# Performance work log

Hardware: AMD Instinct MI355X
Metric: run time of the kernel (lower is better)

The kernel has to match this reference:

```python
import jax, jax.numpy as jnp
import numpy as np

OUT_F, IN_F = 4096, 4096
BITS = 4
B, S = 4, 2048


def setup_inputs() -> dict:
    key = jax.random.key(0)
    k_x, k_cb, k_rot, k_b, k_idx = jax.random.split(key, 5)
    x = jax.random.normal(k_x, (B, S, IN_F), dtype=jnp.float32)
    # per-coordinate codebook indices for each weight row (int, constant)
    indices = jax.random.randint(k_idx, (OUT_F, IN_F), 0, 2 ** BITS, dtype=jnp.int32)
    # scalar codebook with 2^bits levels
    codebook = jax.random.normal(k_cb, (2 ** BITS,), dtype=jnp.float32)
    # random rotation Pi (d x d); faithful math only needs it orthogonal-ish
    rotation_matrix = jax.random.normal(k_rot, (IN_F, IN_F), dtype=jnp.float32) / np.sqrt(IN_F)
    bias = jax.random.normal(k_b, (OUT_F,), dtype=jnp.float32)
    return {"x": x, "indices": indices, "codebook": codebook,
            "rotation_matrix": rotation_matrix, "bias": bias}


def reference(x, indices, codebook, rotation_matrix, bias):
    # Dequantize: look up codewords per coordinate in rotated space, then
    # undo the rotation: W = C[idx] @ Pi^T  -> [out_features, in_features]
    rotated = codebook[indices]                      # [O, D] gather
    weight = jnp.einsum('od,kd->ok', rotated, rotation_matrix)  # rotated @ Pi^T
    # F.linear(x, W, bias) = x @ W^T + bias
    out = jnp.einsum('bsd,od->bso', x, weight) + bias
    return out
```

## Files before the change

kernel.cpp:

```cpp
#include <hip/hip_runtime.h>
#include <hip/hip_bf16.h>


typedef __attribute__((ext_vector_type(8))) __bf16 bf16x8;
typedef __attribute__((ext_vector_type(4))) float f32x4;

#define GLOAD_LDS16(g, l)                                                        \
  __builtin_amdgcn_global_load_lds((__attribute__((address_space(1))) void*)(g), \
                                   (__attribute__((address_space(3))) void*)(l), \
                                   16, 0, 0)

#define SB() __builtin_amdgcn_sched_barrier(0)


__global__ __launch_bounds__(256) void cvt_f32_bf16(const float* __restrict__ in,
                                                    __hip_bfloat16* __restrict__ out, int n4) {
  int i = blockIdx.x * 256 + threadIdx.x;
  if (i >= n4) return;
  float4 v = *(const float4*)(in + (size_t)i * 4);
  union { __hip_bfloat16 h[4]; ushort4 u; } o;
  o.h[0] = __float2bfloat16(v.x);
  o.h[1] = __float2bfloat16(v.y);
  o.h[2] = __float2bfloat16(v.z);
  o.h[3] = __float2bfloat16(v.w);
  *(ushort4*)((unsigned short*)out + (size_t)i * 4) = o.u;
}

__global__ __launch_bounds__(256) void dequant_bf16(const int* __restrict__ idx,
                                                    const float* __restrict__ cb,
                                                    __hip_bfloat16* __restrict__ out, int n4) {
  __shared__ __hip_bfloat16 scb[16];
  if (threadIdx.x < 16) scb[threadIdx.x] = __float2bfloat16(cb[threadIdx.x]);
  __syncthreads();
  int i = blockIdx.x * 256 + threadIdx.x;
  if (i >= n4) return;
  int4 v = *(const int4*)(idx + (size_t)i * 4);
  union { __hip_bfloat16 h[4]; ushort4 u; } o;
  o.h[0] = scb[v.x & 15];
  o.h[1] = scb[v.y & 15];
  o.h[2] = scb[v.z & 15];
  o.h[3] = scb[v.w & 15];
  *(ushort4*)((unsigned short*)out + (size_t)i * 4) = o.u;
}


template <bool OUT_BF16>
__global__ __launch_bounds__(512, 2) void gemm256(const __hip_bfloat16* __restrict__ A,
                                                  const __hip_bfloat16* __restrict__ B,
                                                  void* __restrict__ Cv,
                                                  const float* __restrict__ bias,
                                                  int M, int N, int K) {
  __shared__ __align__(16) char smem[131072];

  const int nbn = N >> 8;
  const int nwg = (M >> 8) * nbn;
  const int bid0 = blockIdx.x;
  const int cpx = nwg >> 3;
  const int bid = (bid0 & 7) * cpx + (bid0 >> 3);
  const int m0 = (bid / nbn) << 8;
  const int n0 = (bid % nbn) << 8;

  const int tid = (int)threadIdx.x;
  const int lane = tid & 63;
  const int w = tid >> 6;
  const int wr = w >> 2;
  const int wc = w & 3;
  const int fr = lane & 15;
  const int fq = lane >> 4;

  const int srow = lane >> 3;
  const int scol = ((lane & 7) ^ srow) << 3;

  const __hip_bfloat16* Ab = A + (size_t)m0 * K;
  const __hip_bfloat16* Bb = B + (size_t)n0 * K;

  const int NT = K >> 6;

  f32x4 acc[8][4];
#pragma unroll
  for (int i = 0; i < 8; ++i)
#pragma unroll
    for (int j = 0; j < 4; ++j) acc[i][j] = (f32x4){0.f, 0.f, 0.f, 0.f};

  auto stage = [&](int s) {
    const int t = s >> 2, kind = s & 3;
    const __hip_bfloat16* g = (kind < 2) ? Ab : Bb;
    char* region = smem + ((kind < 2) ? 0 : 65536) + (t & 1) * 32768 + (kind & 1) * 16384;
    const int grow = (kind & 1) * 128 + w * 16 + srow;
    const int k0 = t << 6;
#pragma unroll
    for (int j = 0; j < 2; ++j)
      GLOAD_LDS16(g + (size_t)(grow + j * 8) * K + (k0 + scol), region + w * 2048 + j * 1024);
  };

  const int fr2 = (fr >> 2) & 1;
  const int fcol = (fq ^ (fr & 3)) << 4;
  const char* pA0 = smem + wr * 16384 + fr * 128 + fcol + 64 * fr2;
  const char* pA1 = smem + wr * 16384 + fr * 128 + fcol + 64 * (1 - fr2);
  const char* pB0 = smem + 65536 + wc * 8192 + fr * 128 + fcol + 64 * fr2;
  const char* pB1 = smem + 65536 + wc * 8192 + fr * 128 + fcol + 64 * (1 - fr2);

#define LDA(BUF, MH, MF, KK) \
  (*(const bf16x8*)(((KK) ? pA1 : pA0) + (BUF) * 32768 + (MH) * 8192 + (MF) * 2048))
#define LDB(BUF, NF, KK) (*(const bf16x8*)(((KK) ? pB1 : pB0) + (BUF) * 32768 + (NF) * 2048))

  stage(0); stage(1); stage(2); stage(3);
  stage(6); stage(7);

  bf16x8 afA[4], afB[4], bk0[4], bk1[4];

#define TILE_BODY(BUF, T)                                                                     \
  {                                                                                           \
    const bool pf1 = ((T) + 1 < NT);                                                          \
    const bool pf2 = ((T) + 2 < NT);                                                          \
                  \
    if ((T) + 1 == NT) {                                                                      \
      asm volatile("s_waitcnt vmcnt(0)" ::: "memory");                                        \
    } else {                                                                                  \
      asm volatile("s_waitcnt vmcnt(4)" ::: "memory");                                        \
    }                                                                                         \
    __builtin_amdgcn_s_barrier();                                                             \
    _Pragma("unroll") for (int mf = 0; mf < 4; ++mf) afA[mf] = LDA(BUF, 0, mf, 0);            \
    _Pragma("unroll") for (int nf = 0; nf < 4; ++nf) bk0[nf] = LDB(BUF, nf, 0);               \
    if (pf1) stage(4 * ((T) + 1) + 0);                                                        \
    asm volatile("s_waitcnt lgkmcnt(0)");                                                     \
    SB();                                                                                     \
    _Pragma("unroll") for (int nf = 0; nf < 4; ++nf)                                          \
        _Pragma("unroll") for (int mf = 0; mf < 4; ++mf)                                      \
            acc[mf][nf] =                                                                     \
                __builtin_amdgcn_mfma_f32_16x16x32_bf16(afA[mf], bk0[nf], acc[mf][nf], 0, 0, 0); \
                                    \
    _Pragma("unroll") for (int mf = 0; mf < 4; ++mf) afB[mf] = LDA(BUF, 0, mf, 1);            \
    _Pragma("unroll") for (int nf = 0; nf < 4; ++nf) bk1[nf] = LDB(BUF, nf, 1);               \
    __builtin_amdgcn_s_barrier();                                                             \
    if (pf1) stage(4 * ((T) + 1) + 1);                                                        \
    asm volatile("s_waitcnt lgkmcnt(0)");                                                     \
    SB();                                                                                     \
    _Pragma("unroll") for (int nf = 0; nf < 4; ++nf)                                          \
        _Pragma("unroll") for (int mf = 0; mf < 4; ++mf)                                      \
            acc[mf][nf] =                                                                     \
                __builtin_amdgcn_mfma_f32_16x16x32_bf16(afB[mf], bk1[nf], acc[mf][nf], 0, 0, 0); \
          \
    _Pragma("unroll") for (int mf = 0; mf < 4; ++mf) afA[mf] = LDA(BUF, 1, mf, 0);            \
    _Pragma("unroll") for (int mf = 0; mf < 4; ++mf) afB[mf] = LDA(BUF, 1, mf, 1);            \
    __builtin_amdgcn_s_barrier();                                                             \
    if (pf2) {                                                                                \
      stage(4 * ((T) + 2) + 2);                                                               \
      stage(4 * ((T) + 2) + 3);                                                               \
    }                                                                                         \
    asm volatile("s_waitcnt lgkmcnt(0)");                                                     \
    SB();                                                                                     \
    _Pragma("unroll") for (int nf = 0; nf < 4; ++nf)                                          \
        _Pragma("unroll") for (int mf = 0; mf < 4; ++mf)                                      \
            acc[4 + mf][nf] = __builtin_amdgcn_mfma_f32_16x16x32_bf16(afA[mf], bk0[nf],       \
                                                                      acc[4 + mf][nf], 0, 0, 0); \
    _Pragma("unroll") for (int nf = 0; nf < 4; ++nf)                                          \
        _Pragma("unroll") for (int mf = 0; mf < 4; ++mf)                                      \
            acc[4 + mf][nf] = __builtin_amdgcn_mfma_f32_16x16x32_bf16(afB[mf], bk1[nf],       \
                                                                      acc[4 + mf][nf], 0, 0, 0); \
  }

  for (int T = 0; T < NT; T += 2) {
    TILE_BODY(0, T);
    TILE_BODY(1, T + 1);
  }
#undef TILE_BODY
#undef LDA
#undef LDB

  if constexpr (OUT_BF16) {
    __hip_bfloat16* C = (__hip_bfloat16*)Cv;
#pragma unroll
    for (int mi = 0; mi < 8; ++mi)
#pragma unroll
      for (int ni = 0; ni < 4; ++ni) {
        const size_t row = (size_t)(m0 + wr * 128 + (mi >> 2) * 64 + (mi & 3) * 16 + fq * 4);
        const int col = n0 + wc * 64 + ni * 16 + fr;
#pragma unroll
        for (int v = 0; v < 4; ++v) C[(row + v) * N + col] = __float2bfloat16(acc[mi][ni][v]);
      }
  } else {
    float* C = (float*)Cv;
    float bv[4];
#pragma unroll
    for (int ni = 0; ni < 4; ++ni) bv[ni] = bias[n0 + wc * 64 + ni * 16 + fr];
#pragma unroll
    for (int mi = 0; mi < 8; ++mi)
#pragma unroll
      for (int ni = 0; ni < 4; ++ni) {
        const size_t row = (size_t)(m0 + wr * 128 + (mi >> 2) * 64 + (mi & 3) * 16 + fq * 4);
        const int col = n0 + wc * 64 + ni * 16 + fr;
#pragma unroll
        for (int v = 0; v < 4; ++v) C[(row + v) * N + col] = acc[mi][ni][v] + bv[ni];
      }
  }
}


extern "C" void kernel_launch(void* const* d_in, const int* in_sizes, int n_in,
                              void* d_out, int out_size, void* d_ws, size_t ws_size,
                              hipStream_t stream) {
  const float* x = (const float*)d_in[0];
  const int* indices = (const int*)d_in[1];
  const float* codebook = (const float*)d_in[2];
  const float* rot = (const float*)d_in[3];
  const float* bias = (const float*)d_in[4];
  float* out = (float*)d_out;

  const int D = 4096, O = 4096;
  const int M = in_sizes[0] / D;

  char* ws = (char*)d_ws;
  __hip_bfloat16* Xb = (__hip_bfloat16*)ws;
  __hip_bfloat16* Rb = (__hip_bfloat16*)(ws + ((size_t)64 << 20));
  __hip_bfloat16* Wr = (__hip_bfloat16*)(ws + ((size_t)96 << 20));
  __hip_bfloat16* Wb = (__hip_bfloat16*)(ws + ((size_t)128 << 20));

  cvt_f32_bf16<<<(M * D / 4 + 255) / 256, 256, 0, stream>>>(x, Xb, M * D / 4);
  cvt_f32_bf16<<<(4096 * 4096 / 4 + 255) / 256, 256, 0, stream>>>(rot, Rb, 4096 * 4096 / 4);
  dequant_bf16<<<(4096 * 4096 / 4 + 255) / 256, 256, 0, stream>>>(indices, codebook, Wr,
                                                                  4096 * 4096 / 4);

  gemm256<true><<<dim3((O / 256) * (4096 / 256)), 512, 0, stream>>>(Wr, Rb, Wb, nullptr, O, 4096,
                                                                    D);
  gemm256<false><<<dim3((M / 256) * (O / 256)), 512, 0, stream>>>(Xb, Wb, out, bias, M, O, 4096);
}
```

Before: 415.5 us.

## Replace 256x256 GEMM tile with 128x128 tile and simpler pipeline

Shrinks each GEMM workgroup from a 256x256 output tile with 8 waves to a 128x128 tile with 4 waves, halves LDS use, and simplifies the prefetch schedule: a full vmcnt(0) wait, then all four stages of the next tile issued at once. This gives more workgroups and higher occupancy, but lowers per-tile data reuse, roughly doubles global/LDS traffic per FLOP, and drops the staggered prefetch overlap.

```diff
diff --git a/kernel.cpp b/kernel.cpp
--- a/kernel.cpp
+++ b/kernel.cpp
@@ -45,26 +45,26 @@
 
 
 template <bool OUT_BF16>
-__global__ __launch_bounds__(512, 2) void gemm256(const __hip_bfloat16* __restrict__ A,
+__global__ __launch_bounds__(256, 2) void gemm128(const __hip_bfloat16* __restrict__ A,
                                                   const __hip_bfloat16* __restrict__ B,
                                                   void* __restrict__ Cv,
                                                   const float* __restrict__ bias,
                                                   int M, int N, int K) {
-  __shared__ __align__(16) char smem[131072];
-
-  const int nbn = N >> 8;
-  const int nwg = (M >> 8) * nbn;
+  __shared__ __align__(16) char smem[65536];
+
+  const int nbn = N >> 7;
+  const int nwg = (M >> 7) * nbn;
   const int bid0 = blockIdx.x;
   const int cpx = nwg >> 3;
   const int bid = (bid0 & 7) * cpx + (bid0 >> 3);
-  const int m0 = (bid / nbn) << 8;
-  const int n0 = (bid % nbn) << 8;
+  const int m0 = (bid / nbn) << 7;
+  const int n0 = (bid % nbn) << 7;
 
   const int tid = (int)threadIdx.x;
   const int lane = tid & 63;
   const int w = tid >> 6;
-  const int wr = w >> 2;
-  const int wc = w & 3;
+  const int wr = w >> 1;
+  const int wc = w & 1;
   const int fr = lane & 15;
   const int fq = lane >> 4;
 
@@ -76,17 +76,17 @@
 
   const int NT = K >> 6;
 
-  f32x4 acc[8][4];
-#pragma unroll
-  for (int i = 0; i < 8; ++i)
+  f32x4 acc[4][4];
+#pragma unroll
+  for (int i = 0; i < 4; ++i)
 #pragma unroll
     for (int j = 0; j < 4; ++j) acc[i][j] = (f32x4){0.f, 0.f, 0.f, 0.f};
 
   auto stage = [&](int s) {
     const int t = s >> 2, kind = s & 3;
     const __hip_bfloat16* g = (kind < 2) ? Ab : Bb;
-    char* region = smem + ((kind < 2) ? 0 : 65536) + (t & 1) * 32768 + (kind & 1) * 16384;
-    const int grow = (kind & 1) * 128 + w * 16 + srow;
+    char* region = smem + ((kind < 2) ? 0 : 32768) + (t & 1) * 16384 + (kind & 1) * 8192;
+    const int grow = (kind & 1) * 64 + w * 16 + srow;
     const int k0 = t << 6;
 #pragma unroll
     for (int j = 0; j < 2; ++j)
@@ -95,69 +95,47 @@
 
   const int fr2 = (fr >> 2) & 1;
   const int fcol = (fq ^ (fr & 3)) << 4;
-  const char* pA0 = smem + wr * 16384 + fr * 128 + fcol + 64 * fr2;
-  const char* pA1 = smem + wr * 16384 + fr * 128 + fcol + 64 * (1 - fr2);
-  const char* pB0 = smem + 65536 + wc * 8192 + fr * 128 + fcol + 64 * fr2;
-  const char* pB1 = smem + 65536 + wc * 8192 + fr * 128 + fcol + 64 * (1 - fr2);
-
-#define LDA(BUF, MH, MF, KK) \
-  (*(const bf16x8*)(((KK) ? pA1 : pA0) + (BUF) * 32768 + (MH) * 8192 + (MF) * 2048))
-#define LDB(BUF, NF, KK) (*(const bf16x8*)(((KK) ? pB1 : pB0) + (BUF) * 32768 + (NF) * 2048))
+  const char* pA0 = smem + wr * 8192 + fr * 128 + fcol + 64 * fr2;
+  const char* pA1 = smem + wr * 8192 + fr * 128 + fcol + 64 * (1 - fr2);
+  const char* pB0 = smem + 32768 + wc * 8192 + fr * 128 + fcol + 64 * fr2;
+  const char* pB1 = smem + 32768 + wc * 8192 + fr * 128 + fcol + 64 * (1 - fr2);
+
+#define LDA(BUF, MF, KK) (*(const bf16x8*)(((KK) ? pA1 : pA0) + (BUF) * 16384 + (MF) * 2048))
+#define LDB(BUF, NF, KK) (*(const bf16x8*)(((KK) ? pB1 : pB0) + (BUF) * 16384 + (NF) * 2048))
 
   stage(0); stage(1); stage(2); stage(3);
-  stage(6); stage(7);
 
   bf16x8 afA[4], afB[4], bk0[4], bk1[4];
 
 #define TILE_BODY(BUF, T)                                                                     \
   {                                                                                           \
     const bool pf1 = ((T) + 1 < NT);                                                          \
-    const bool pf2 = ((T) + 2 < NT);                                                          \
-                  \
-    if ((T) + 1 == NT) {                                                                      \
-      asm volatile("s_waitcnt vmcnt(0)" ::: "memory");                                        \
-    } else {                                                                                  \
-      asm volatile("s_waitcnt vmcnt(4)" ::: "memory");                                        \
+                                         \
+    asm volatile("s_waitcnt vmcnt(0)" ::: "memory");                                          \
+    __builtin_amdgcn_s_barrier();                                                             \
+    _Pragma("unroll") for (int mf = 0; mf < 4; ++mf) afA[mf] = LDA(BUF, mf, 0);               \
+    _Pragma("unroll") for (int nf = 0; nf < 4; ++nf) bk0[nf] = LDB(BUF, nf, 0);               \
+    if (pf1) {                                                                                \
+      stage(4 * ((T) + 1) + 0);                                                               \
+      stage(4 * ((T) + 1) + 1);                                                               \
+      stage(4 * ((T) + 1) + 2);                                                               \
+      stage(4 * ((T) + 1) + 3);                                                               \
     }                                                                                         \
-    __builtin_amdgcn_s_barrier();                                                             \
-    _Pragma("unroll") for (int mf = 0; mf < 4; ++mf) afA[mf] = LDA(BUF, 0, mf, 0);            \
-    _Pragma("unroll") for (int nf = 0; nf < 4; ++nf) bk0[nf] = LDB(BUF, nf, 0);               \
-    if (pf1) stage(4 * ((T) + 1) + 0);                                                        \
     asm volatile("s_waitcnt lgkmcnt(0)");                                                     \
     SB();                                                                                     \
     _Pragma("unroll") for (int nf = 0; nf < 4; ++nf)                                          \
         _Pragma("unroll") for (int mf = 0; mf < 4; ++mf)                                      \
             acc[mf][nf] =                                                                     \
                 __builtin_amdgcn_mfma_f32_16x16x32_bf16(afA[mf], bk0[nf], acc[mf][nf], 0, 0, 0); \
-                                    \
-    _Pragma("unroll") for (int mf = 0; mf < 4; ++mf) afB[mf] = LDA(BUF, 0, mf, 1);            \
+     \
+    _Pragma("unroll") for (int mf = 0; mf < 4; ++mf) afB[mf] = LDA(BUF, mf, 1);               \
     _Pragma("unroll") for (int nf = 0; nf < 4; ++nf) bk1[nf] = LDB(BUF, nf, 1);               \
-    __builtin_amdgcn_s_barrier();                                                             \
-    if (pf1) stage(4 * ((T) + 1) + 1);                                                        \
     asm volatile("s_waitcnt lgkmcnt(0)");                                                     \
     SB();                                                                                     \
     _Pragma("unroll") for (int nf = 0; nf < 4; ++nf)                                          \
         _Pragma("unroll") for (int mf = 0; mf < 4; ++mf)                                      \
             acc[mf][nf] =                                                                     \
                 __builtin_amdgcn_mfma_f32_16x16x32_bf16(afB[mf], bk1[nf], acc[mf][nf], 0, 0, 0); \
-          \
-    _Pragma("unroll") for (int mf = 0; mf < 4; ++mf) afA[mf] = LDA(BUF, 1, mf, 0);            \
-    _Pragma("unroll") for (int mf = 0; mf < 4; ++mf) afB[mf] = LDA(BUF, 1, mf, 1);            \
-    __builtin_amdgcn_s_barrier();                                                             \
-    if (pf2) {                                                                                \
-      stage(4 * ((T) + 2) + 2);                                                               \
-      stage(4 * ((T) + 2) + 3);                                                               \
-    }                                                                                         \
-    asm volatile("s_waitcnt lgkmcnt(0)");                                                     \
-    SB();                                                                                     \
-    _Pragma("unroll") for (int nf = 0; nf < 4; ++nf)                                          \
-        _Pragma("unroll") for (int mf = 0; mf < 4; ++mf)                                      \
-            acc[4 + mf][nf] = __builtin_amdgcn_mfma_f32_16x16x32_bf16(afA[mf], bk0[nf],       \
-                                                                      acc[4 + mf][nf], 0, 0, 0); \
-    _Pragma("unroll") for (int nf = 0; nf < 4; ++nf)                                          \
-        _Pragma("unroll") for (int mf = 0; mf < 4; ++mf)                                      \
-            acc[4 + mf][nf] = __builtin_amdgcn_mfma_f32_16x16x32_bf16(afB[mf], bk1[nf],       \
-                                                                      acc[4 + mf][nf], 0, 0, 0); \
   }
 
   for (int T = 0; T < NT; T += 2) {
@@ -171,10 +149,10 @@
   if constexpr (OUT_BF16) {
     __hip_bfloat16* C = (__hip_bfloat16*)Cv;
 #pragma unroll
-    for (int mi = 0; mi < 8; ++mi)
+    for (int mi = 0; mi < 4; ++mi)
 #pragma unroll
       for (int ni = 0; ni < 4; ++ni) {
-        const size_t row = (size_t)(m0 + wr * 128 + (mi >> 2) * 64 + (mi & 3) * 16 + fq * 4);
+        const size_t row = (size_t)(m0 + wr * 64 + mi * 16 + fq * 4);
         const int col = n0 + wc * 64 + ni * 16 + fr;
 #pragma unroll
         for (int v = 0; v < 4; ++v) C[(row + v) * N + col] = __float2bfloat16(acc[mi][ni][v]);
@@ -185,10 +163,10 @@
 #pragma unroll
     for (int ni = 0; ni < 4; ++ni) bv[ni] = bias[n0 + wc * 64 + ni * 16 + fr];
 #pragma unroll
-    for (int mi = 0; mi < 8; ++mi)
+    for (int mi = 0; mi < 4; ++mi)
 #pragma unroll
       for (int ni = 0; ni < 4; ++ni) {
-        const size_t row = (size_t)(m0 + wr * 128 + (mi >> 2) * 64 + (mi & 3) * 16 + fq * 4);
+        const size_t row = (size_t)(m0 + wr * 64 + mi * 16 + fq * 4);
         const int col = n0 + wc * 64 + ni * 16 + fr;
 #pragma unroll
         for (int v = 0; v < 4; ++v) C[(row + v) * N + col] = acc[mi][ni][v] + bv[ni];
@@ -221,7 +199,7 @@
   dequant_bf16<<<(4096 * 4096 / 4 + 255) / 256, 256, 0, stream>>>(indices, codebook, Wr,
                                                                   4096 * 4096 / 4);
 
-  gemm256<true><<<dim3((O / 256) * (4096 / 256)), 512, 0, stream>>>(Wr, Rb, Wb, nullptr, O, 4096,
+  gemm128<true><<<dim3((O / 128) * (4096 / 128)), 256, 0, stream>>>(Wr, Rb, Wb, nullptr, O, 4096,
                                                                     D);
-  gemm256<false><<<dim3((M / 256) * (O / 256)), 512, 0, stream>>>(Xb, Wb, out, bias, M, O, 4096);
-}
+  gemm128<false><<<dim3((M / 128) * (O / 128)), 256, 0, stream>>>(Xb, Wb, out, bias, M, O, 4096);
+}
```

Measured after the change: 522.0 us. 1.26x slower.
